# Kernel tuning notes

Hardware: AMD Instinct MI355X
Metric: run time of the kernel (lower is better)

## Reference

```python
import jax, jax.numpy as jnp
import numpy as np

NUM_HEADS = 12
DIM = 768
HW = 64                # h = w = 64, seqlen = 4096
L = HW * HW
HIDDEN = 4 * DIM


def _dwconv(img, w, b):
    # img: (C, H, W); w: (C, 1, 3, 3) depthwise; b: (C,)
    y = jax.lax.conv_general_dilated(
        img[None], w, window_strides=(1, 1), padding=((1, 1), (1, 1)),
        feature_group_count=img.shape[0],
        dimension_numbers=('NCHW', 'OIHW', 'NCHW'))[0]
    return y + b[:, None, None]


def _ln(t, w, b, eps=1e-5):
    mu = t.mean(-1, keepdims=True)
    var = ((t - mu) ** 2).mean(-1, keepdims=True)
    return (t - mu) / jnp.sqrt(var + eps) * w + b


def _rope_cos_sin(H, W, D, base=10000.0):
    # MLLA-style axial 2D RoPE over feature dim D: k_max = D // (2*ndim)
    k_max = D // 4
    theta = 1.0 / (base ** (jnp.arange(k_max, dtype=jnp.float32) / k_max))
    ax = jnp.arange(H, dtype=jnp.float32)[:, None, None] * theta  # (H,1,k)
    ay = jnp.arange(W, dtype=jnp.float32)[None, :, None] * theta  # (1,W,k)
    angles = jnp.concatenate([
        jnp.broadcast_to(ax, (H, W, k_max)),
        jnp.broadcast_to(ay, (H, W, k_max))], axis=-1)  # (H, W, D/2)
    return jnp.cos(angles), jnp.sin(angles)


def _rope_apply(t, cos, sin):
    # t: (H, W, D); rotate consecutive feature pairs (complex mult)
    H, W, D = t.shape
    t2 = t.reshape(H, W, D // 2, 2)
    x0, x1 = t2[..., 0], t2[..., 1]
    return jnp.stack([x0 * cos - x1 * sin, x0 * sin + x1 * cos], axis=-1).reshape(H, W, D)


def setup_inputs() -> dict:
    key = jax.random.key(0)
    ks = jax.random.split(key, 18)
    s = 0.02
    f32 = jnp.float32
    return {
        'x': jax.random.normal(ks[0], (L, DIM), f32),
        'cpe1_w': jax.random.normal(ks[1], (DIM, 1, 3, 3), f32) * s,
        'cpe1_b': jnp.zeros((DIM,), f32),
        'norm1_w': jnp.ones((DIM,), f32),
        'norm1_b': jnp.zeros((DIM,), f32),
        'qk_w': jax.random.normal(ks[2], (2 * DIM, DIM), f32) * s,
        'qk_b': jnp.zeros((2 * DIM,), f32),
        'lepe_w': jax.random.normal(ks[3], (DIM, 1, 3, 3), f32) * s,
        'lepe_b': jnp.zeros((DIM,), f32),
        'cpe2_w': jax.random.normal(ks[4], (DIM, 1, 3, 3), f32) * s,
        'cpe2_b': jnp.zeros((DIM,), f32),
        'norm2_w': jnp.ones((DIM,), f32),
        'norm2_b': jnp.zeros((DIM,), f32),
        'fc1_w': jax.random.normal(ks[5], (HIDDEN, DIM), f32) * s,
        'fc1_b': jnp.zeros((HIDDEN,), f32),
        'fc2_w': jax.random.normal(ks[6], (DIM, HIDDEN), f32) * s,
        'fc2_b': jnp.zeros((DIM,), f32),
    }


def reference(x, cpe1_w, cpe1_b, norm1_w, norm1_b, qk_w, qk_b, lepe_w, lepe_b,
              cpe2_w, cpe2_b, norm2_w, norm2_b, fc1_w, fc1_b, fc2_w, fc2_b):
    n, C = x.shape          # (4096, 768)
    Hh = Ww = HW
    h, d = NUM_HEADS, C // NUM_HEADS

    # --- CPE1 + norm1 ---
    x1 = x + _dwconv(x.T.reshape(C, Hh, Ww), cpe1_w, cpe1_b).reshape(C, n).T
    x1 = _ln(x1, norm1_w, norm1_b)

    # --- LinearAttention (ELU+1 kernel, RoPE, LePE) ---
    qk = x1 @ qk_w.T + qk_b                                   # (n, 2C)
    q = qk[:, :C].reshape(n, h, d).transpose(1, 0, 2)          # (h, n, d)
    k = qk[:, C:].reshape(n, h, d).transpose(1, 0, 2)
    v = x1.reshape(n, h, d).transpose(1, 0, 2)
    q = jax.nn.elu(q) + 1.0
    k = jax.nn.elu(k) + 1.0

    cos, sin = _rope_cos_sin(Hh, Ww, C)
    to2d = lambda t: t.transpose(1, 0, 2).reshape(Hh, Ww, C)
    from2d = lambda t: t.reshape(n, h, d).transpose(1, 0, 2)
    q_rope = from2d(_rope_apply(to2d(q), cos, sin))
    k_rope = from2d(_rope_apply(to2d(k), cos, sin))

    z = 1.0 / (jnp.einsum('hnd,hd->hn', q, k.mean(axis=1)) + 1e-6)
    scale = n ** (-0.5)
    kv = jnp.einsum('hnd,hne->hde', k_rope * scale, v * scale)  # (h, d, d)
    a = jnp.einsum('hnd,hde->hne', q_rope, kv) * z[..., None]   # (h, n, d)
    a = a.transpose(1, 0, 2).reshape(n, C)

    lepe_out = _dwconv(x1.T.reshape(C, Hh, Ww), lepe_w, lepe_b).reshape(C, n).T
    x1 = a + lepe_out

    # --- residual + CPE2 + MLP ---
    x = x + x1
    x = x + _dwconv(x.T.reshape(C, Hh, Ww), cpe2_w, cpe2_b).reshape(C, n).T
    y = _ln(x, norm2_w, norm2_b)
    y = jax.nn.silu(y @ fc1_w.T + fc1_b) @ fc2_w.T + fc2_b
    return x + y
```

## Files before the change

kernel.cpp:

```cpp
#include <hip/hip_runtime.h>
#include <hip/hip_bf16.h>
#include <stdint.h>

#define DIM 768
#define NTOK 4096

typedef __bf16 bf16x8_t __attribute__((ext_vector_type(8)));
typedef float f32x4_t __attribute__((ext_vector_type(4)));
typedef unsigned short u16x8 __attribute__((ext_vector_type(8)));

__device__ __forceinline__ float bf2f(unsigned short u) {
    union { unsigned int i; float f; } v; v.i = ((unsigned int)u) << 16; return v.f;
}
__device__ __forceinline__ unsigned short f2bf(float f) {
    union { float f; unsigned int i; } v; v.f = f;
    unsigned int x = v.i;
    unsigned int r = x + 0x7fffu + ((x >> 16) & 1u);
    return (unsigned short)(r >> 16);
}
__device__ __forceinline__ u16x8 pack8(const float4& a, const float4& b) {
    u16x8 o;
    o[0] = f2bf(a.x); o[1] = f2bf(a.y); o[2] = f2bf(a.z); o[3] = f2bf(a.w);
    o[4] = f2bf(b.x); o[5] = f2bf(b.y); o[6] = f2bf(b.z); o[7] = f2bf(b.w);
    return o;
}

__device__ __forceinline__ void wait_lgkm0() {
    asm volatile("s_waitcnt lgkmcnt(0)" ::: "memory");
    __builtin_amdgcn_sched_barrier(0);
}

__global__ __launch_bounds__(256) void prep(
    const float* __restrict__ qkw, const float* __restrict__ fc1w, const float* __restrict__ fc2w,
    unsigned short* __restrict__ oqk, unsigned short* __restrict__ ofc1,
    unsigned short* __restrict__ ofc2, float* __restrict__ zbuf)
{
    const int b = blockIdx.x, t = threadIdx.x;
    const float* src; unsigned short* dst; int rel;
    if (b < 1152)      { src = qkw;  dst = oqk;  rel = b; }
    else if (b < 3456) { src = fc1w; dst = ofc1; rel = b - 1152; }
    else if (b < 5760) { src = fc2w; dst = ofc2; rel = b - 3456; }
    else { zbuf[(b - 5760) * 256 + t] = 0.f; return; }
    int i = rel * 1024 + t * 4;
    float4 v = *(const float4*)&src[i];
    ushort4 o;
    o.x = f2bf(v.x); o.y = f2bf(v.y); o.z = f2bf(v.z); o.w = f2bf(v.w);
    *(ushort4*)&dst[i] = o;
}

template<int DO_LN, int BASE_BF16, int CIN_BF16, int PRE_BF16>
__global__ __launch_bounds__(256) void conv_ln(
    const void* __restrict__ base_, const void* __restrict__ cin_,
    const float* __restrict__ cw, const float* __restrict__ cb,
    const float* __restrict__ lnw, const float* __restrict__ lnb,
    void* __restrict__ pre_out, unsigned short* __restrict__ lnb16_out)
{
    const int n = blockIdx.x;
    const int hh = n >> 6, ww = n & 63;
    const int t = threadIdx.x;
    float s[3];
#pragma unroll
    for (int i = 0; i < 3; i++) {
        int c = t + i * 256;
        float acc = cb[c];
#pragma unroll
        for (int dh = -1; dh <= 1; dh++) {
            int h2 = hh + dh;
            if ((unsigned)h2 < 64u) {
#pragma unroll
                for (int dw = -1; dw <= 1; dw++) {
                    int w2 = ww + dw;
                    if ((unsigned)w2 < 64u) {
                        size_t idx = (size_t)(h2 * 64 + w2) * DIM + c;
                        float cv = CIN_BF16 ? bf2f(((const unsigned short*)cin_)[idx])
                                            : ((const float*)cin_)[idx];
                        acc = fmaf(cv, cw[c * 9 + (dh + 1) * 3 + (dw + 1)], acc);
                    }
                }
            }
        }
        size_t idx = (size_t)n * DIM + c;
        float v = (BASE_BF16 ? bf2f(((const unsigned short*)base_)[idx])
                             : ((const float*)base_)[idx]) + acc;
        s[i] = v;
        if (pre_out) {
            if (PRE_BF16) ((unsigned short*)pre_out)[idx] = f2bf(v);
            else          ((float*)pre_out)[idx] = v;
        }
    }
    if (DO_LN) {
        float s1 = s[0] + s[1] + s[2];
        float s2 = s[0] * s[0] + s[1] * s[1] + s[2] * s[2];
#pragma unroll
        for (int o = 32; o; o >>= 1) { s1 += __shfl_xor(s1, o); s2 += __shfl_xor(s2, o); }
        __shared__ float red[8];
        int w = t >> 6, lane = t & 63;
        if (lane == 0) { red[w * 2] = s1; red[w * 2 + 1] = s2; }
        __syncthreads();
        s1 = red[0] + red[2] + red[4] + red[6];
        s2 = red[1] + red[3] + red[5] + red[7];
        float mean = s1 * (1.f / 768.f);
        float var = s2 * (1.f / 768.f) - mean * mean;
        float rstd = rsqrtf(var + 1e-5f);
#pragma unroll
        for (int i = 0; i < 3; i++) {
            int c = t + i * 256;
            float vn = (s[i] - mean) * rstd * lnw[c] + lnb[c];
            lnb16_out[(size_t)n * DIM + c] = f2bf(vn);
        }
    }
}

template<int BM, int BN, int NBX, int PR, int PC, int SILU, int OUTBF16, int ADD, int ADDBF16, int ROPE>
__global__ __launch_bounds__(512, 2) void gemm_bt(
    const unsigned short* __restrict__ A, const unsigned short* __restrict__ B,
    const float* __restrict__ bias, const void* __restrict__ addsrc,
    void* __restrict__ outp,
    unsigned short* __restrict__ qr, unsigned short* __restrict__ krs,
    unsigned short* __restrict__ qpre, float* __restrict__ ksum,
    int N, int K)
{
    constexpr int WC  = BN / 64;
    constexpr int WR  = 8 / WC;
    constexpr int RB  = BM / WR;
    constexpr int MF  = RB / 16;
    constexpr int ACW = BM / 64;
    constexpr int BCW = BN / 64;
    constexpr int XC  = NBX / PC;
    __shared__ __align__(128) unsigned short aL[2][BM * 64];
    __shared__ __align__(128) unsigned short bL[2][BN * 64];

    const int xcd = blockIdx.x & 7, local = blockIdx.x >> 3;
    const int brow = (xcd / XC) * PR + local / PC;
    const int bcol = (xcd % XC) * PC + local % PC;
    const int t = threadIdx.x, w = t >> 6, lane = t & 63;
    const int wr = w / WC, wc = w % WC;
    const int lr = lane >> 3;
    const int sl = lane & 7;
    const int swz = ((sl ^ lr) << 4) + lr * 128;

    const unsigned short* aSrc[ACW];
#pragma unroll
    for (int i = 0; i < ACW; i++)
        aSrc[i] = A + (size_t)(brow * BM + (w * ACW + i) * 8 + lr) * K + sl * 8;
    const unsigned short* bSrc[BCW];
#pragma unroll
    for (int i = 0; i < BCW; i++)
        bSrc[i] = B + (size_t)(bcol * BN + (w * BCW + i) * 8 + lr) * K + sl * 8;

    f32x4_t acc[MF][4];
#pragma unroll
    for (int m = 0; m < MF; m++)
#pragma unroll
        for (int n = 0; n < 4; n++) acc[m][n] = (f32x4_t){0.f, 0.f, 0.f, 0.f};

    u16x8 rA[ACW], rB[BCW];
#define LOADT(k0) do { \
    _Pragma("unroll") for (int i_ = 0; i_ < ACW; i_++) rA[i_] = *(const u16x8*)(aSrc[i_] + (k0)); \
    _Pragma("unroll") for (int i_ = 0; i_ < BCW; i_++) rB[i_] = *(const u16x8*)(bSrc[i_] + (k0)); } while (0)
#define WRITET(buf) do { \
    _Pragma("unroll") for (int i_ = 0; i_ < ACW; i_++) \
        *(u16x8*)((char*)aL[buf] + (w * ACW + i_) * 1024 + swz) = rA[i_]; \
    _Pragma("unroll") for (int i_ = 0; i_ < BCW; i_++) \
        *(u16x8*)((char*)bL[buf] + (w * BCW + i_) * 1024 + swz) = rB[i_]; } while (0)

    const int nt = K >> 6;
    LOADT(0);

    const int fr = lane & 15;
    const int xr = (fr & 7) << 4;
    const int cbase = (lane >> 4) << 4;
    for (int tt = 0; tt < nt; ++tt) {
        WRITET(tt & 1);
        if (tt + 1 < nt) LOADT((tt + 1) * 64);
        wait_lgkm0();
        __builtin_amdgcn_s_barrier();
        const char* ab = (const char*)aL[tt & 1];
        const char* bb = (const char*)bL[tt & 1];
#pragma unroll
        for (int ks = 0; ks < 2; ks++) {
            bf16x8_t af[MF], bfv[4];
#pragma unroll
            for (int m = 0; m < MF; m++)
                af[m] = *(const bf16x8_t*)(ab + (((wr * RB + m * 16 + fr) * 128 + cbase + ks * 64) ^ xr));
#pragma unroll
            for (int n = 0; n < 4; n++)
                bfv[n] = *(const bf16x8_t*)(bb + (((wc * 64 + n * 16 + fr) * 128 + cbase + ks * 64) ^ xr));
            __builtin_amdgcn_s_setprio(1);
#pragma unroll
            for (int m = 0; m < MF; m++)
#pragma unroll
                for (int n = 0; n < 4; n++)
                    acc[m][n] = __builtin_amdgcn_mfma_f32_16x16x32_bf16(af[m], bfv[n], acc[m][n], 0, 0, 0);
            __builtin_amdgcn_s_setprio(0);
        }
        wait_lgkm0();
        __builtin_amdgcn_s_barrier();
    }
#undef LOADT
#undef WRITET

    const int rb = brow * BM + wr * RB + (lane >> 4) * 4;
    const int cb = bcol * BN + wc * 64 + fr;

    if constexpr (ROPE) {
        const bool isq = (bcol < 6);
        const bool use_h = ((bcol % 6) < 3);
#pragma unroll
        for (int n = 0; n < 4; n++) {
            int col = cb + n * 16;
            float bs = bias[col];
            int cm = isq ? col : col - 768;
            int p = cm >> 1;
            int pmv = use_h ? p : p - 192;
            float th = __expf(-(float)pmv * (9.210340371976184f / 192.f));
            float kssum = 0.f;
#pragma unroll
            for (int m = 0; m < MF; m++) {
#pragma unroll
                for (int j = 0; j < 4; j++) {
                    int row = rb + m * 16 + j;
                    float v = acc[m][n][j] + bs;
                    float e = v > 0.f ? v + 1.f : __expf(v);
                    float pe = __shfl_xor(e, 1);
                    float pos = use_h ? (float)(row >> 6) : (float)(row & 63);
                    float sa, ca;
                    __sincosf(pos * th, &sa, &ca);
                    float rot = (fr & 1) ? (pe * sa + e * ca) : (e * ca - pe * sa);
                    if (isq) {
                        qr[(size_t)row * 768 + col] = f2bf(rot);
                        qpre[(size_t)row * 768 + col] = f2bf(e);
                    } else {
                        krs[(size_t)row * 768 + cm] = f2bf(rot * 0.015625f);
                        kssum += e;
                    }
                }
            }
            if (!isq) {
                kssum += __shfl_xor(kssum, 16);
                kssum += __shfl_xor(kssum, 32);
                if (lane < 16) atomicAdd(&ksum[cm], kssum);
            }
        }
    } else {
#pragma unroll
        for (int n = 0; n < 4; n++) {
            int col = cb + n * 16;
            float bs = bias ? bias[col] : 0.f;
#pragma unroll
            for (int m = 0; m < MF; m++) {
#pragma unroll
                for (int j = 0; j < 4; j++) {
                    int row = rb + m * 16 + j;
                    float v = acc[m][n][j] + bs;
                    if (SILU) v = v / (1.f + __expf(-v));
                    if (ADD) {
                        size_t idx = (size_t)row * N + col;
                        v += ADDBF16 ? bf2f(((const unsigned short*)addsrc)[idx])
                                     : ((const float*)addsrc)[idx];
                    }
                    if (OUTBF16) ((unsigned short*)outp)[(size_t)row * N + col] = f2bf(v);
                    else ((float*)outp)[(size_t)row * N + col] = v;
                }
            }
        }
    }
}

__global__ __launch_bounds__(256) void kv_accum(
    const unsigned short* __restrict__ krs, const unsigned short* __restrict__ x1b,
    float* __restrict__ kvout)
{
    const int chunk = blockIdx.x, h = blockIdx.y;
    const int n0 = chunk * 128;
    __shared__ float kl[128][64];
    __shared__ float vl[128][64];
    const int t = threadIdx.x;
    const int r = t >> 1, cs = (t & 1) * 32;
#pragma unroll
    for (int j = 0; j < 32; j += 8) {
        u16x8 kk = *(const u16x8*)&krs[(size_t)(n0 + r) * DIM + h * 64 + cs + j];
        u16x8 vv = *(const u16x8*)&x1b[(size_t)(n0 + r) * DIM + h * 64 + cs + j];
#pragma unroll
        for (int e = 0; e < 8; e++) {
            kl[r][cs + j + e] = bf2f(kk[e]);
            vl[r][cs + j + e] = bf2f(vv[e]) * 0.015625f;
        }
    }
    __syncthreads();
    const int td = t >> 4, te = t & 15;
    float a[4][4] = {};
    for (int nn = 0; nn < 128; nn++) {
        f32x4_t kd = *(const f32x4_t*)&kl[nn][td * 4];
        f32x4_t ve = *(const f32x4_t*)&vl[nn][te * 4];
#pragma unroll
        for (int i = 0; i < 4; i++)
#pragma unroll
            for (int j = 0; j < 4; j++)
                a[i][j] = fmaf(kd[i], ve[j], a[i][j]);
    }
#pragma unroll
    for (int i = 0; i < 4; i++)
#pragma unroll
        for (int j = 0; j < 4; j++)
            atomicAdd(&kvout[h * 4096 + (te * 4 + j) * 64 + (td * 4 + i)], a[i][j]);
}

__global__ __launch_bounds__(256) void attn_lepe(
    const unsigned short* __restrict__ qr, const unsigned short* __restrict__ qpre,
    const float* __restrict__ ksum, const float* __restrict__ kvT,
    const float* __restrict__ x, const unsigned short* __restrict__ x1b,
    const float* __restrict__ lepe_w, const float* __restrict__ lepe_b,
    unsigned short* __restrict__ x2b)
{
    const int h = blockIdx.y;
    const int chunk = blockIdx.x;
    const int n0 = chunk * 128;
    const int c0 = h * 64;
    const int R0 = chunk * 2;
    const int t = threadIdx.x, w = t >> 6, lane = t & 63;
    __shared__ __align__(128) unsigned short kvL[64 * 64];
    __shared__ __align__(128) unsigned short x1L[4][64][64];
    __shared__ float zl[128];
    __shared__ float kmL[64];

    {
        const int e = t >> 2, db = (t & 3) * 16;
        const float* src = &kvT[h * 4096 + e * 64 + db];
        float4 v0 = *(const float4*)&src[0];
        float4 v1 = *(const float4*)&src[4];
        float4 v2 = *(const float4*)&src[8];
        float4 v3 = *(const float4*)&src[12];
        int s0 = ((db >> 3) + 0) ^ (e & 7);
        int s1 = ((db >> 3) + 1) ^ (e & 7);
        *(u16x8*)((char*)kvL + e * 128 + s0 * 16) = pack8(v0, v1);
        *(u16x8*)((char*)kvL + e * 128 + s1 * 16) = pack8(v2, v3);
    }
    {
        const int r = t >> 6, ww = t & 63;
        const int rr = R0 - 1 + r;
        const bool ok = (unsigned)rr < 64u;
        const unsigned short* sp = &x1b[(size_t)(rr * 64 + ww) * DIM + c0];
#pragma unroll
        for (int jj = 0; jj < 8; jj++) {
            u16x8 vv;
            if (ok) vv = *(const u16x8*)(sp + jj * 8);
            else    vv = (u16x8)(0);
            *(u16x8*)&x1L[r][ww][jj * 8] = vv;
        }
    }
    if (t < 64) kmL[t] = ksum[h * 64 + t] * (1.f / 4096.f);
    __syncthreads();

    {
        const int tok = t >> 1, half = (t & 1) * 32;
        const unsigned short* qp = &qpre[(size_t)(n0 + tok) * DIM + c0 + half];
        float zs = 0.f;
#pragma unroll
        for (int j = 0; j < 32; j += 8) {
            u16x8 qv = *(const u16x8*)&qp[j];
#pragma unroll
            for (int e = 0; e < 8; e++) zs = fmaf(bf2f(qv[e]), kmL[half + j + e], zs);
        }
        zs += __shfl_xor(zs, 1);
        if ((t & 1) == 0) zl[tok] = 1.f / (zs + 1e-6f);
    }
    __syncthreads();

    const int fr = lane & 15;
    const int kc = (lane >> 4) * 8;
    const unsigned short* qbase = qr + (size_t)(n0 + w * 32 + fr) * DIM + c0 + kc;

    f32x4_t acc[2][4];
#pragma unroll
    for (int m = 0; m < 2; m++)
#pragma unroll
        for (int n = 0; n < 4; n++) acc[m][n] = (f32x4_t){0.f, 0.f, 0.f, 0.f};

#pragma unroll
    for (int ks = 0; ks < 2; ks++) {
        bf16x8_t af[2], bfv[4];
#pragma unroll
        for (int m = 0; m < 2; m++)
            af[m] = *(const bf16x8_t*)(qbase + (size_t)m * 16 * DIM + ks * 32);
#pragma unroll
        for (int n = 0; n < 4; n++) {
            int e = n * 16 + fr;
            int slot = (ks * 4 + (lane >> 4)) ^ (e & 7);
            bfv[n] = *(const bf16x8_t*)((const char*)kvL + e * 128 + slot * 16);
        }
#pragma unroll
        for (int m = 0; m < 2; m++)
#pragma unroll
            for (int n = 0; n < 4; n++)
                acc[m][n] = __builtin_amdgcn_mfma_f32_16x16x32_bf16(af[m], bfv[n], acc[m][n], 0, 0, 0);
    }

    const int r4 = (lane >> 4) * 4;
#pragma unroll
    for (int n = 0; n < 4; n++) {
        const int cc = n * 16 + fr;
        const int c = c0 + cc;
        float w9[9];
#pragma unroll
        for (int q2 = 0; q2 < 9; q2++) w9[q2] = lepe_w[c * 9 + q2];
        const float lb = lepe_b[c];
#pragma unroll
        for (int m = 0; m < 2; m++) {
#pragma unroll
            for (int j = 0; j < 4; j++) {
                const int tr = w * 32 + m * 16 + r4 + j;
                float av = acc[m][n][j] * zl[tr];
                const int ww = tr & 63;
                const int rbase = (tr >> 6) + 1;
                float conv = 0.f;
#pragma unroll
                for (int dh = -1; dh <= 1; dh++) {
#pragma unroll
                    for (int dw = -1; dw <= 1; dw++) {
                        int w2 = ww + dw;
                        if ((unsigned)w2 < 64u)
                            conv = fmaf(bf2f(x1L[rbase + dh][w2][cc]),
                                        w9[(dh + 1) * 3 + (dw + 1)], conv);
                    }
                }
                float xr2 = x[(size_t)(n0 + tr) * DIM + c];
                x2b[(size_t)(n0 + tr) * DIM + c] = f2bf(xr2 + av + conv + lb);
            }
        }
    }
}

extern "C" void kernel_launch(void* const* d_in, const int* in_sizes, int n_in,
                              void* d_out, int out_size, void* d_ws, size_t ws_size,
                              hipStream_t stream) {
    (void)in_sizes; (void)n_in; (void)out_size; (void)ws_size;
    const float* x       = (const float*)d_in[0];
    const float* cpe1_w  = (const float*)d_in[1];
    const float* cpe1_b  = (const float*)d_in[2];
    const float* norm1_w = (const float*)d_in[3];
    const float* norm1_b = (const float*)d_in[4];
    const float* qk_w    = (const float*)d_in[5];
    const float* qk_b    = (const float*)d_in[6];
    const float* lepe_w  = (const float*)d_in[7];
    const float* lepe_b  = (const float*)d_in[8];
    const float* cpe2_w  = (const float*)d_in[9];
    const float* cpe2_b  = (const float*)d_in[10];
    const float* norm2_w = (const float*)d_in[11];
    const float* norm2_b = (const float*)d_in[12];
    const float* fc1_w   = (const float*)d_in[13];
    const float* fc1_b   = (const float*)d_in[14];
    const float* fc2_w   = (const float*)d_in[15];
    const float* fc2_b   = (const float*)d_in[16];
    char* ws = (char*)d_ws;

    constexpr size_t o_qkwb  = 0;
    constexpr size_t o_fc1wb = o_qkwb  + (size_t)1536 * 768 * 2;
    constexpr size_t o_fc2wb = o_fc1wb + (size_t)3072 * 768 * 2;
    constexpr size_t o_x1b   = o_fc2wb + (size_t)768 * 3072 * 2;
    constexpr size_t o_big   = o_x1b   + (size_t)4096 * 768 * 2;
    constexpr size_t o_qr    = o_big   + (size_t)4096 * 3072 * 2;
    constexpr size_t o_krs   = o_qr    + (size_t)4096 * 768 * 2;
    constexpr size_t o_qpre  = o_krs   + (size_t)4096 * 768 * 2;
    constexpr size_t o_ksum  = o_qpre  + (size_t)4096 * 768 * 2;
    constexpr size_t o_kv    = o_ksum  + (size_t)768 * 4;
    constexpr size_t o_x3b   = o_kv    + (size_t)12 * 64 * 64 * 4;
    constexpr size_t o_yb    = o_x3b   + (size_t)4096 * 768 * 2;

    unsigned short* x2b = (unsigned short*)(ws + o_big);
    unsigned short* h_b = (unsigned short*)(ws + o_big);

    prep<<<5955, 256, 0, stream>>>(qk_w, fc1_w, fc2_w,
                                   (unsigned short*)(ws + o_qkwb), (unsigned short*)(ws + o_fc1wb),
                                   (unsigned short*)(ws + o_fc2wb), (float*)(ws + o_ksum));
    conv_ln<1, 0, 0, 0><<<4096, 256, 0, stream>>>(x, x, cpe1_w, cpe1_b, norm1_w, norm1_b,
                                                  nullptr, (unsigned short*)(ws + o_x1b));
    gemm_bt<256, 128, 12, 2, 12, 0, 0, 0, 0, 1><<<192, 512, 0, stream>>>(
        (const unsigned short*)(ws + o_x1b), (const unsigned short*)(ws + o_qkwb),
        qk_b, nullptr, nullptr,
        (unsigned short*)(ws + o_qr), (unsigned short*)(ws + o_krs),
        (unsigned short*)(ws + o_qpre), (float*)(ws + o_ksum),
        1536, 768);
    kv_accum<<<dim3(32, 12), 256, 0, stream>>>((const unsigned short*)(ws + o_krs),
                                               (const unsigned short*)(ws + o_x1b),
                                               (float*)(ws + o_kv));
    attn_lepe<<<dim3(32, 12), 256, 0, stream>>>((const unsigned short*)(ws + o_qr),
                                                (const unsigned short*)(ws + o_qpre),
                                                (const float*)(ws + o_ksum), (const float*)(ws + o_kv),
                                                x, (const unsigned short*)(ws + o_x1b),
                                                lepe_w, lepe_b, x2b);
    conv_ln<1, 1, 1, 1><<<4096, 256, 0, stream>>>(x2b, x2b, cpe2_w, cpe2_b, norm2_w, norm2_b,
                                                  (void*)(ws + o_x3b), (unsigned short*)(ws + o_yb));
    gemm_bt<256, 128, 24, 4, 12, 1, 1, 0, 0, 0><<<384, 512, 0, stream>>>(
        (const unsigned short*)(ws + o_yb), (const unsigned short*)(ws + o_fc1wb),
        fc1_b, nullptr, h_b, nullptr, nullptr, nullptr, nullptr,
        3072, 768);
    gemm_bt<128, 128, 6, 4, 6, 0, 0, 1, 1, 0><<<192, 512, 0, stream>>>(
        h_b, (const unsigned short*)(ws + o_fc2wb),
        fc2_b, (const void*)(ws + o_x3b), d_out, nullptr, nullptr, nullptr, nullptr,
        768, 3072);
}
```

Before: 209.5 us.

## Double-buffer register prefetch and overlap LDS writes with MFMA compute

```diff
diff --git a/kernel.cpp b/kernel.cpp
--- a/kernel.cpp
+++ b/kernel.cpp
@@ -154,51 +154,68 @@
 #pragma unroll
         for (int n = 0; n < 4; n++) acc[m][n] = (f32x4_t){0.f, 0.f, 0.f, 0.f};
 
-    u16x8 rA[ACW], rB[BCW];
-#define LOADT(k0) do { \
-    _Pragma("unroll") for (int i_ = 0; i_ < ACW; i_++) rA[i_] = *(const u16x8*)(aSrc[i_] + (k0)); \
-    _Pragma("unroll") for (int i_ = 0; i_ < BCW; i_++) rB[i_] = *(const u16x8*)(bSrc[i_] + (k0)); } while (0)
-#define WRITET(buf) do { \
+    u16x8 rA0[ACW], rB0[BCW], rA1[ACW], rB1[BCW];
+#define LOADT0(k0) do { \
+    _Pragma("unroll") for (int i_ = 0; i_ < ACW; i_++) rA0[i_] = *(const u16x8*)(aSrc[i_] + (k0)); \
+    _Pragma("unroll") for (int i_ = 0; i_ < BCW; i_++) rB0[i_] = *(const u16x8*)(bSrc[i_] + (k0)); } while (0)
+#define LOADT1(k0) do { \
+    _Pragma("unroll") for (int i_ = 0; i_ < ACW; i_++) rA1[i_] = *(const u16x8*)(aSrc[i_] + (k0)); \
+    _Pragma("unroll") for (int i_ = 0; i_ < BCW; i_++) rB1[i_] = *(const u16x8*)(bSrc[i_] + (k0)); } while (0)
+#define WRITET0(buf) do { \
     _Pragma("unroll") for (int i_ = 0; i_ < ACW; i_++) \
-        *(u16x8*)((char*)aL[buf] + (w * ACW + i_) * 1024 + swz) = rA[i_]; \
+        *(u16x8*)((char*)aL[buf] + (w * ACW + i_) * 1024 + swz) = rA0[i_]; \
     _Pragma("unroll") for (int i_ = 0; i_ < BCW; i_++) \
-        *(u16x8*)((char*)bL[buf] + (w * BCW + i_) * 1024 + swz) = rB[i_]; } while (0)
-
-    const int nt = K >> 6;
-    LOADT(0);
+        *(u16x8*)((char*)bL[buf] + (w * BCW + i_) * 1024 + swz) = rB0[i_]; } while (0)
+#define WRITET1(buf) do { \
+    _Pragma("unroll") for (int i_ = 0; i_ < ACW; i_++) \
+        *(u16x8*)((char*)aL[buf] + (w * ACW + i_) * 1024 + swz) = rA1[i_]; \
+    _Pragma("unroll") for (int i_ = 0; i_ < BCW; i_++) \
+        *(u16x8*)((char*)bL[buf] + (w * BCW + i_) * 1024 + swz) = rB1[i_]; } while (0)
 
     const int fr = lane & 15;
     const int xr = (fr & 7) << 4;
     const int cbase = (lane >> 4) << 4;
-    for (int tt = 0; tt < nt; ++tt) {
-        WRITET(tt & 1);
-        if (tt + 1 < nt) LOADT((tt + 1) * 64);
+#define COMPUTE(buf) do { \
+    const char* ab_ = (const char*)aL[buf]; \
+    const char* bb_ = (const char*)bL[buf]; \
+    _Pragma("unroll") for (int ks = 0; ks < 2; ks++) { \
+        bf16x8_t af[MF], bfv[4]; \
+        _Pragma("unroll") for (int m = 0; m < MF; m++) \
+            af[m] = *(const bf16x8_t*)(ab_ + (((wr * RB + m * 16 + fr) * 128 + cbase + ks * 64) ^ xr)); \
+        _Pragma("unroll") for (int n = 0; n < 4; n++) \
+            bfv[n] = *(const bf16x8_t*)(bb_ + (((wc * 64 + n * 16 + fr) * 128 + cbase + ks * 64) ^ xr)); \
+        __builtin_amdgcn_s_setprio(1); \
+        _Pragma("unroll") for (int m = 0; m < MF; m++) \
+            _Pragma("unroll") for (int n = 0; n < 4; n++) \
+                acc[m][n] = __builtin_amdgcn_mfma_f32_16x16x32_bf16(af[m], bfv[n], acc[m][n], 0, 0, 0); \
+        __builtin_amdgcn_s_setprio(0); \
+    } } while (0)
+
+    const int nt = K >> 6;
+    LOADT0(0);
+    LOADT1(64);
+    WRITET0(0);
+    LOADT0(128);
+    wait_lgkm0();
+    __builtin_amdgcn_s_barrier();
+
+    for (int tt = 0; tt < nt; tt += 2) {
+        WRITET1(1);
+        if (tt + 3 < nt) LOADT1((tt + 3) * 64);
+        COMPUTE(0);
         wait_lgkm0();
         __builtin_amdgcn_s_barrier();
-        const char* ab = (const char*)aL[tt & 1];
-        const char* bb = (const char*)bL[tt & 1];
-#pragma unroll
-        for (int ks = 0; ks < 2; ks++) {
-            bf16x8_t af[MF], bfv[4];
-#pragma unroll
-            for (int m = 0; m < MF; m++)
-                af[m] = *(const bf16x8_t*)(ab + (((wr * RB + m * 16 + fr) * 128 + cbase + ks * 64) ^ xr));
-#pragma unroll
-            for (int n = 0; n < 4; n++)
-                bfv[n] = *(const bf16x8_t*)(bb + (((wc * 64 + n * 16 + fr) * 128 + cbase + ks * 64) ^ xr));
-            __builtin_amdgcn_s_setprio(1);
-#pragma unroll
-            for (int m = 0; m < MF; m++)
-#pragma unroll
-                for (int n = 0; n < 4; n++)
-                    acc[m][n] = __builtin_amdgcn_mfma_f32_16x16x32_bf16(af[m], bfv[n], acc[m][n], 0, 0, 0);
-            __builtin_amdgcn_s_setprio(0);
-        }
+        if (tt + 2 < nt) WRITET0(0);
+        if (tt + 4 < nt) LOADT0((tt + 4) * 64);
+        COMPUTE(1);
         wait_lgkm0();
         __builtin_amdgcn_s_barrier();
     }
-#undef LOADT
-#undef WRITET
+#undef LOADT0
+#undef LOADT1
+#undef WRITET0
+#undef WRITET1
+#undef COMPUTE
 
     const int rb = brow * BM + wr * RB + (lane >> 4) * 4;
     const int cb = bcol * BN + wc * 64 + fr;
```

Result: faster. 204.9 us (-2.2%).

## Use direct global-to-LDS loads and smaller 128x64 GEMM tiles with 4 waves

Applied to the files above, without the earlier changes.

```diff
diff --git a/kernel.cpp b/kernel.cpp
--- a/kernel.cpp
+++ b/kernel.cpp
@@ -25,9 +25,9 @@
     return o;
 }
 
-__device__ __forceinline__ void wait_lgkm0() {
-    asm volatile("s_waitcnt lgkmcnt(0)" ::: "memory");
-    __builtin_amdgcn_sched_barrier(0);
+__device__ __forceinline__ void gload_lds16(const void* g, void* l) {
+    __builtin_amdgcn_global_load_lds((const __attribute__((address_space(1))) void*)g,
+                                     (__attribute__((address_space(3))) void*)l, 16, 0, 0);
 }
 
 __global__ __launch_bounds__(256) void prep(
@@ -111,8 +111,8 @@
     }
 }
 
-template<int BM, int BN, int NBX, int PR, int PC, int SILU, int OUTBF16, int ADD, int ADDBF16, int ROPE>
-__global__ __launch_bounds__(512, 2) void gemm_bt(
+template<int BM, int NBX, int PR, int PC, int SILU, int OUTBF16, int ADD, int ADDBF16, int ROPE>
+__global__ __launch_bounds__(256, 3) void gemm_bt(
     const unsigned short* __restrict__ A, const unsigned short* __restrict__ B,
     const float* __restrict__ bias, const void* __restrict__ addsrc,
     void* __restrict__ outp,
@@ -120,12 +120,11 @@
     unsigned short* __restrict__ qpre, float* __restrict__ ksum,
     int N, int K)
 {
-    constexpr int WC  = BN / 64;
-    constexpr int WR  = 8 / WC;
-    constexpr int RB  = BM / WR;
+    constexpr int BN  = 64;
+    constexpr int RB  = BM / 4;
     constexpr int MF  = RB / 16;
-    constexpr int ACW = BM / 64;
-    constexpr int BCW = BN / 64;
+    constexpr int ACW = BM / 32;
+    constexpr int BCW = BN / 32;
     constexpr int XC  = NBX / PC;
     __shared__ __align__(128) unsigned short aL[2][BM * 64];
     __shared__ __align__(128) unsigned short bL[2][BN * 64];
@@ -134,10 +133,8 @@
     const int brow = (xcd / XC) * PR + local / PC;
     const int bcol = (xcd % XC) * PC + local % PC;
     const int t = threadIdx.x, w = t >> 6, lane = t & 63;
-    const int wr = w / WC, wc = w % WC;
     const int lr = lane >> 3;
-    const int sl = lane & 7;
-    const int swz = ((sl ^ lr) << 4) + lr * 128;
+    const int sl = (lane & 7) ^ lr;
 
     const unsigned short* aSrc[ACW];
 #pragma unroll
@@ -154,27 +151,21 @@
 #pragma unroll
         for (int n = 0; n < 4; n++) acc[m][n] = (f32x4_t){0.f, 0.f, 0.f, 0.f};
 
-    u16x8 rA[ACW], rB[BCW];
-#define LOADT(k0) do { \
-    _Pragma("unroll") for (int i_ = 0; i_ < ACW; i_++) rA[i_] = *(const u16x8*)(aSrc[i_] + (k0)); \
-    _Pragma("unroll") for (int i_ = 0; i_ < BCW; i_++) rB[i_] = *(const u16x8*)(bSrc[i_] + (k0)); } while (0)
-#define WRITET(buf) do { \
+#define STAGE(buf, k0) do { \
     _Pragma("unroll") for (int i_ = 0; i_ < ACW; i_++) \
-        *(u16x8*)((char*)aL[buf] + (w * ACW + i_) * 1024 + swz) = rA[i_]; \
+        gload_lds16(aSrc[i_] + (k0), &aL[buf][(w * ACW + i_) * 512]); \
     _Pragma("unroll") for (int i_ = 0; i_ < BCW; i_++) \
-        *(u16x8*)((char*)bL[buf] + (w * BCW + i_) * 1024 + swz) = rB[i_]; } while (0)
+        gload_lds16(bSrc[i_] + (k0), &bL[buf][(w * BCW + i_) * 512]); } while (0)
 
     const int nt = K >> 6;
-    LOADT(0);
+    STAGE(0, 0);
+    __syncthreads();
 
     const int fr = lane & 15;
     const int xr = (fr & 7) << 4;
     const int cbase = (lane >> 4) << 4;
     for (int tt = 0; tt < nt; ++tt) {
-        WRITET(tt & 1);
-        if (tt + 1 < nt) LOADT((tt + 1) * 64);
-        wait_lgkm0();
-        __builtin_amdgcn_s_barrier();
+        if (tt + 1 < nt) STAGE((tt + 1) & 1, (tt + 1) * 64);
         const char* ab = (const char*)aL[tt & 1];
         const char* bb = (const char*)bL[tt & 1];
 #pragma unroll
@@ -182,10 +173,10 @@
             bf16x8_t af[MF], bfv[4];
 #pragma unroll
             for (int m = 0; m < MF; m++)
-                af[m] = *(const bf16x8_t*)(ab + (((wr * RB + m * 16 + fr) * 128 + cbase + ks * 64) ^ xr));
+                af[m] = *(const bf16x8_t*)(ab + (((w * RB + m * 16 + fr) * 128 + cbase + ks * 64) ^ xr));
 #pragma unroll
             for (int n = 0; n < 4; n++)
-                bfv[n] = *(const bf16x8_t*)(bb + (((wc * 64 + n * 16 + fr) * 128 + cbase + ks * 64) ^ xr));
+                bfv[n] = *(const bf16x8_t*)(bb + (((n * 16 + fr) * 128 + cbase + ks * 64) ^ xr));
             __builtin_amdgcn_s_setprio(1);
 #pragma unroll
             for (int m = 0; m < MF; m++)
@@ -194,18 +185,16 @@
                     acc[m][n] = __builtin_amdgcn_mfma_f32_16x16x32_bf16(af[m], bfv[n], acc[m][n], 0, 0, 0);
             __builtin_amdgcn_s_setprio(0);
         }
-        wait_lgkm0();
-        __builtin_amdgcn_s_barrier();
-    }
-#undef LOADT
-#undef WRITET
-
-    const int rb = brow * BM + wr * RB + (lane >> 4) * 4;
-    const int cb = bcol * BN + wc * 64 + fr;
+        __syncthreads();
+    }
+#undef STAGE
+
+    const int rb = brow * BM + w * RB + (lane >> 4) * 4;
+    const int cb = bcol * BN + fr;
 
     if constexpr (ROPE) {
-        const bool isq = (bcol < 6);
-        const bool use_h = ((bcol % 6) < 3);
+        const bool isq = (bcol < 12);
+        const bool use_h = ((bcol % 12) < 6);
 #pragma unroll
         for (int n = 0; n < 4; n++) {
             int col = cb + n * 16;
@@ -475,7 +464,7 @@
                                    (unsigned short*)(ws + o_fc2wb), (float*)(ws + o_ksum));
     conv_ln<1, 0, 0, 0><<<4096, 256, 0, stream>>>(x, x, cpe1_w, cpe1_b, norm1_w, norm1_b,
                                                   nullptr, (unsigned short*)(ws + o_x1b));
-    gemm_bt<256, 128, 12, 2, 12, 0, 0, 0, 0, 1><<<192, 512, 0, stream>>>(
+    gemm_bt<128, 24, 8, 12, 0, 0, 0, 0, 1><<<768, 256, 0, stream>>>(
         (const unsigned short*)(ws + o_x1b), (const unsigned short*)(ws + o_qkwb),
         qk_b, nullptr, nullptr,
         (unsigned short*)(ws + o_qr), (unsigned short*)(ws + o_krs),
@@ -491,11 +480,11 @@
                                                 lepe_w, lepe_b, x2b);
     conv_ln<1, 1, 1, 1><<<4096, 256, 0, stream>>>(x2b, x2b, cpe2_w, cpe2_b, norm2_w, norm2_b,
                                                   (void*)(ws + o_x3b), (unsigned short*)(ws + o_yb));
-    gemm_bt<256, 128, 24, 4, 12, 1, 1, 0, 0, 0><<<384, 512, 0, stream>>>(
+    gemm_bt<128, 48, 16, 12, 1, 1, 0, 0, 0><<<1536, 256, 0, stream>>>(
         (const unsigned short*)(ws + o_yb), (const unsigned short*)(ws + o_fc1wb),
         fc1_b, nullptr, h_b, nullptr, nullptr, nullptr, nullptr,
         3072, 768);
-    gemm_bt<128, 128, 6, 4, 6, 0, 0, 1, 1, 0><<<192, 512, 0, stream>>>(
+    gemm_bt<128, 12, 8, 6, 0, 0, 1, 1, 0><<<384, 256, 0, stream>>>(
         h_b, (const unsigned short*)(ws + o_fc2wb),
         fc2_b, (const void*)(ws + o_x3b), d_out, nullptr, nullptr, nullptr, nullptr,
         768, 3072);
```

Measured after the change: 205.7 us. Within noise of the previous version (-1.8%).
